# Kernel optimization log

Hardware: AMD Instinct MI355X
Metric: run time of the kernel (lower is better)

Reference implementation:

```python
import jax, jax.numpy as jnp
import numpy as np

B, IN_CH, OUT_CH, ZDIM, KSZ, WH = 16, 64, 64, 64, 3, 32
T, K = 32768, 128


def setup_inputs() -> dict:
    key = jax.random.key(0)
    ks = jax.random.split(key, 10)
    bound = float(np.sqrt(6.0 / OUT_CH))
    return {
        "x": jax.random.normal(ks[0], (B, IN_CH, T), jnp.float32),
        "z": jax.random.normal(ks[1], (B, ZDIM, K), jnp.float32),
        # weight_model: conv1x1(ZDIM->WH), ReLU, conv1x1(WH->IN_CH*OUT_CH*KSZ)
        "wm1": jax.random.normal(ks[2], (WH, ZDIM), jnp.float32) * 0.1,
        "wb1": jnp.zeros((WH,), jnp.float32),
        "wm2": jax.random.normal(ks[3], (IN_CH * OUT_CH * KSZ, WH), jnp.float32) * 0.02,
        "wb2": jnp.zeros((IN_CH * OUT_CH * KSZ,), jnp.float32),
        # bias_model: conv1x1(ZDIM->WH), ReLU, conv1x1(WH->OUT_CH)
        "bm1": jax.random.normal(ks[4], (WH, ZDIM), jnp.float32) * 0.1,
        "bb1": jnp.zeros((WH,), jnp.float32),
        "bm2": jax.random.normal(ks[5], (OUT_CH, WH), jnp.float32) * 0.1,
        "bb2": jnp.zeros((OUT_CH,), jnp.float32),
        # residual / skip 1x1 convs (uniform init per module)
        "rw": jax.random.uniform(ks[6], (OUT_CH, OUT_CH), jnp.float32, -bound, bound),
        "rb": jnp.zeros((OUT_CH,), jnp.float32),
        "sw": jax.random.uniform(ks[7], (OUT_CH, OUT_CH), jnp.float32, -bound, bound),
        "sb": jnp.zeros((OUT_CH,), jnp.float32),
    }


def reference(x, z, wm1, wb1, wm2, wb2, bm1, bb1, bm2, bb2, rw, rb, sw, sb):
    Bq, Cin, Tq = x.shape
    Kq = z.shape[-1]
    S = Tq // Kq  # samples per segment

    # hypernet: per-segment weights, shape (B, Cin*KSZ*OUT_CH, K)
    h = jax.nn.relu(jnp.einsum('hz,bzk->bhk', wm1, z) + wb1[None, :, None])
    w = jnp.einsum('oh,bhk->bok', wm2, h) + wb2[None, :, None]
    # (B, Cin*KSZ, OUT_CH, K) -> (B, K, KSZ, Cin, OUT_CH)
    w = w.reshape(Bq, KSZ, Cin, OUT_CH, Kq).transpose(0, 4, 1, 2, 3)
    # torch cat concatenates KSZ identical copies of x along channels (the
    # dilation shifts are absent in the source), so summing the weight over
    w_eff = w.sum(axis=2)  # (B, K, Cin, OUT_CH)

    hb = jax.nn.relu(jnp.einsum('hz,bzk->bhk', bm1, z) + bb1[None, :, None])
    b = jnp.einsum('oh,bhk->bok', bm2, hb) + bb2[None, :, None]  # (B, OUT_CH, K)
    b = b.transpose(0, 2, 1)  # (B, K, OUT_CH)

    # per-segment batched matmul
    xr = x.transpose(0, 2, 1).reshape(Bq, Kq, S, Cin)
    y = jnp.einsum('bksi,bkio->bkso', xr, w_eff) + b[:, :, None, :]
    y = jnp.sin(y.reshape(Bq, Tq, OUT_CH).transpose(0, 2, 1))  # (B, OUT_CH, T)

    residual = jnp.einsum('oc,bct->bot', rw, y) + rb[None, :, None]
    skip = jnp.einsum('oc,bct->bot', sw, y) + sb[None, :, None]
    return (residual + x) / 2, skip
```

## Files before the change

kernel.cpp:

```cpp
#include <hip/hip_runtime.h>
#include <hip/hip_bf16.h>

#define B_    16
#define CIN   64
#define COUT  64
#define ZD    64
#define WHID  32
#define TT    32768
#define KK    128
#define SS    256

__global__ void k_tapsum(const float* __restrict__ wm2, float* __restrict__ wm2s) {
    int i = blockIdx.x * 256 + threadIdx.x;
    if (i < 4096 * 32)
        wm2s[i] = wm2[i] + wm2[i + 131072] + wm2[i + 262144];
}

__global__ __launch_bounds__(256) void k_hyper_small(
    const float* __restrict__ z,
    const float* __restrict__ wm1, const float* __restrict__ wb1,
    const float* __restrict__ bm1, const float* __restrict__ bb1,
    const float* __restrict__ bm2, const float* __restrict__ bb2,
    float* __restrict__ ws_h, float* __restrict__ ws_bias)
{
    __shared__ float hb[8][32];
    const int tid = threadIdx.x;
    const int seg = tid >> 5, w = tid & 31;
    const int bk = blockIdx.x * 8 + seg;
    const int b = bk >> 7, k = bk & 127;
    const float* zp = z + b * ZD * KK + k;

    float hv = wb1[w], hbv = bb1[w];
    #pragma unroll
    for (int zz = 0; zz < 64; ++zz) {
        float zv = zp[zz * KK];
        hv  += wm1[w * 64 + zz] * zv;
        hbv += bm1[w * 64 + zz] * zv;
    }
    hv  = fmaxf(hv, 0.f);
    hbv = fmaxf(hbv, 0.f);
    ws_h[bk * 32 + w] = hv;
    hb[seg][w] = hbv;
    __syncthreads();

    #pragma unroll
    for (int t = 0; t < 2; ++t) {
        int o = w + t * 32;
        float acc = bb2[o];
        #pragma unroll
        for (int hh = 0; hh < 32; ++hh)
            acc += bm2[o * 32 + hh] * hb[seg][hh];
        ws_bias[bk * 64 + o] = acc;
    }
}

__global__ __launch_bounds__(256) void k_weff(
    const float* __restrict__ wm2s, const float* __restrict__ wb2,
    const float* __restrict__ ws_h, float* __restrict__ ws_w)
{
    const int tid = threadIdx.x;
    const int wave = tid >> 6, lane = tid & 63;
    const int bk0 = blockIdx.x * 16 + wave * 4;

    float hreg[4][32];
    #pragma unroll
    for (int q = 0; q < 4; ++q) {
        #pragma unroll
        for (int hh = 0; hh < 32; ++hh)
            hreg[q][hh] = ws_h[(bk0 + q) * 32 + hh];
    }

    for (int jj = 0; jj < 64; ++jj) {
        int j = jj * 64 + lane;
        float4 row[8];
        const float4* rp = (const float4*)(wm2s + j * 32);
        #pragma unroll
        for (int q = 0; q < 8; ++q) row[q] = rp[q];
        float wb = wb2[j] + wb2[j + 4096] + wb2[j + 8192];
        const float* rowf = (const float*)row;
        #pragma unroll
        for (int q = 0; q < 4; ++q) {
            float acc = wb;
            #pragma unroll
            for (int hh = 0; hh < 32; ++hh)
                acc += rowf[hh] * hreg[q][hh];
            ws_w[(size_t)(bk0 + q) * 4096 + j] = acc;
        }
    }
}

__global__ __launch_bounds__(256, 2) void k_main(
    const float* __restrict__ x,
    const float* __restrict__ ws_w, const float* __restrict__ ws_bias,
    const float* __restrict__ rw, const float* __restrict__ rb,
    const float* __restrict__ sw, const float* __restrict__ sb,
    float* __restrict__ out)
{
    __shared__ float U[8192];
    __shared__ unsigned short ybuf[64][256];

    const int tid = threadIdx.x;
    const int bk = blockIdx.x;
    const int b = bk >> 7, k = bk & 127;
    const int tbase = k * SS;
    const int sg = tid & 63, og = tid >> 6;
    const int s0 = sg * 4, o0 = og * 16;
    float4* U4 = (float4*)U;

    {
        const float4* Wg = (const float4*)(ws_w + (size_t)bk * 4096);
        #pragma unroll
        for (int r = 0; r < 4; ++r) U4[tid + 256 * r] = Wg[tid + 256 * r];
        if (tid < 64) U[4096 + tid] = ws_bias[bk * 64 + tid];
    }
    __syncthreads();

    float acc[4][16];
    #pragma unroll
    for (int e = 0; e < 4; ++e)
        #pragma unroll
        for (int v = 0; v < 16; ++v) acc[e][v] = 0.f;

    const float* xs = x + (size_t)b * CIN * TT + tbase + s0;
    #pragma unroll 8
    for (int i = 0; i < 64; ++i) {
        float4 xv = *(const float4*)(xs + (size_t)i * TT);
        #pragma unroll
        for (int q = 0; q < 4; ++q) {
            float4 wq = U4[i * 16 + og * 4 + q];
            float wv[4] = {wq.x, wq.y, wq.z, wq.w};
            #pragma unroll
            for (int e2 = 0; e2 < 4; ++e2) {
                acc[0][q * 4 + e2] += xv.x * wv[e2];
                acc[1][q * 4 + e2] += xv.y * wv[e2];
                acc[2][q * 4 + e2] += xv.z * wv[e2];
                acc[3][q * 4 + e2] += xv.w * wv[e2];
            }
        }
    }
    #pragma unroll
    for (int v = 0; v < 16; ++v) {
        int o = o0 + v;
        float bo = U[4096 + o];
        unsigned int us[4];
        #pragma unroll
        for (int e = 0; e < 4; ++e) {
            float yv = __sinf(acc[e][v] + bo);
            unsigned int u = __float_as_uint(yv);
            u += 0x7fffu + ((u >> 16) & 1u);
            us[e] = u >> 16;
        }
        uint2 pk;
        pk.x = us[0] | (us[1] << 16);
        pk.y = us[2] | (us[3] << 16);
        *(uint2*)&ybuf[o][s0] = pk;
    }
    __syncthreads();

    #pragma unroll
    for (int r = 0; r < 16; ++r) {
        int e = tid + 256 * r;
        int o = e >> 6, c = e & 63;
        U[c * 64 + o]        = rw[e];
        U[4096 + c * 64 + o] = sw[e];
    }
    __syncthreads();

    float ar[4][16], asx[4][16];
    #pragma unroll
    for (int e = 0; e < 4; ++e)
        #pragma unroll
        for (int v = 0; v < 16; ++v) { ar[e][v] = 0.f; asx[e][v] = 0.f; }

    #pragma unroll 4
    for (int c = 0; c < 64; ++c) {
        uint2 yu = *(const uint2*)&ybuf[c][s0];
        float yv[4];
        yv[0] = __uint_as_float(yu.x << 16);
        yv[1] = __uint_as_float(yu.x & 0xffff0000u);
        yv[2] = __uint_as_float(yu.y << 16);
        yv[3] = __uint_as_float(yu.y & 0xffff0000u);
        #pragma unroll
        for (int q = 0; q < 4; ++q) {
            float4 rq = U4[c * 16 + og * 4 + q];
            float4 sq = U4[1024 + c * 16 + og * 4 + q];
            float rv[4] = {rq.x, rq.y, rq.z, rq.w};
            float sv[4] = {sq.x, sq.y, sq.z, sq.w};
            #pragma unroll
            for (int e2 = 0; e2 < 4; ++e2) {
                #pragma unroll
                for (int e = 0; e < 4; ++e) {
                    ar[e][q * 4 + e2]  += yv[e] * rv[e2];
                    asx[e][q * 4 + e2] += yv[e] * sv[e2];
                }
            }
        }
    }

    float* resp = out;
    float* skpp = out + (size_t)B_ * COUT * TT;
    #pragma unroll
    for (int v = 0; v < 16; ++v) {
        int o = o0 + v;
        size_t off = (size_t)(b * COUT + o) * TT + tbase + s0;
        float4 xo = *(const float4*)(x + off);
        float rbv = rb[o], sbv = sb[o];
        float4 ro, so;
        ro.x = (ar[0][v] + rbv + xo.x) * 0.5f;
        ro.y = (ar[1][v] + rbv + xo.y) * 0.5f;
        ro.z = (ar[2][v] + rbv + xo.z) * 0.5f;
        ro.w = (ar[3][v] + rbv + xo.w) * 0.5f;
        so.x = asx[0][v] + sbv;
        so.y = asx[1][v] + sbv;
        so.z = asx[2][v] + sbv;
        so.w = asx[3][v] + sbv;
        *(float4*)(resp + off) = ro;
        *(float4*)(skpp + off) = so;
    }
}

extern "C" void kernel_launch(void* const* d_in, const int* in_sizes, int n_in,
                              void* d_out, int out_size, void* d_ws, size_t ws_size,
                              hipStream_t stream) {
    const float* x   = (const float*)d_in[0];
    const float* z   = (const float*)d_in[1];
    const float* wm1 = (const float*)d_in[2];
    const float* wb1 = (const float*)d_in[3];
    const float* wm2 = (const float*)d_in[4];
    const float* wb2 = (const float*)d_in[5];
    const float* bm1 = (const float*)d_in[6];
    const float* bb1 = (const float*)d_in[7];
    const float* bm2 = (const float*)d_in[8];
    const float* bb2 = (const float*)d_in[9];
    const float* rw  = (const float*)d_in[10];
    const float* rb  = (const float*)d_in[11];
    const float* sw  = (const float*)d_in[12];
    const float* sb  = (const float*)d_in[13];
    float* out = (float*)d_out;

    float* ws      = (float*)d_ws;
    float* ws_wm2s = ws;
    float* ws_h    = ws + 131072;
    float* ws_bias = ws + 196608;
    float* ws_w    = ws + 327680;

    hipLaunchKernelGGL(k_tapsum, dim3(512), dim3(256), 0, stream, wm2, ws_wm2s);
    hipLaunchKernelGGL(k_hyper_small, dim3(256), dim3(256), 0, stream,
                       z, wm1, wb1, bm1, bb1, bm2, bb2, ws_h, ws_bias);
    hipLaunchKernelGGL(k_weff, dim3(128), dim3(256), 0, stream,
                       ws_wm2s, wb2, ws_h, ws_w);
    hipLaunchKernelGGL(k_main, dim3(2048), dim3(256), 0, stream,
                       x, ws_w, ws_bias, rw, rb, sw, sb, out);
}
```

Before: 596.3 us.

## Stage x through LDS with cooperative prefetch and packed FMA accumulation

After: 1.027 ms. +72.2%, slower.

```diff
diff --git a/kernel.cpp b/kernel.cpp
--- a/kernel.cpp
+++ b/kernel.cpp
@@ -9,6 +9,9 @@
 #define TT    32768
 #define KK    128
 #define SS    256
+
+typedef float f2 __attribute__((ext_vector_type(2)));
+typedef float f4 __attribute__((ext_vector_type(4)));
 
 __global__ void k_tapsum(const float* __restrict__ wm2, float* __restrict__ wm2s) {
     int i = blockIdx.x * 256 + threadIdx.x;
@@ -97,7 +100,7 @@
     float* __restrict__ out)
 {
     __shared__ float U[8192];
-    __shared__ unsigned short ybuf[64][256];
+    __shared__ __align__(16) unsigned short ybuf[64][256];
 
     const int tid = threadIdx.x;
     const int bk = blockIdx.x;
@@ -105,39 +108,73 @@
     const int tbase = k * SS;
     const int sg = tid & 63, og = tid >> 6;
     const int s0 = sg * 4, o0 = og * 16;
-    float4* U4 = (float4*)U;
+    f4* U4 = (f4*)U;
+    f4* xch = (f4*)&ybuf[0][0];
 
     {
-        const float4* Wg = (const float4*)(ws_w + (size_t)bk * 4096);
+        const f4* Wg = (const f4*)(ws_w + (size_t)bk * 4096);
         #pragma unroll
         for (int r = 0; r < 4; ++r) U4[tid + 256 * r] = Wg[tid + 256 * r];
         if (tid < 64) U[4096 + tid] = ws_bias[bk * 64 + tid];
     }
-    __syncthreads();
-
-    float acc[4][16];
+
+    const float* xg = x + (size_t)b * CIN * TT + tbase + s0;
+    f4 pend0 = *(const f4*)(xg + (size_t)(0  + og) * TT);
+    f4 pend1 = *(const f4*)(xg + (size_t)(4  + og) * TT);
+    f4 pend2 = *(const f4*)(xg + (size_t)(8  + og) * TT);
+    f4 pend3 = *(const f4*)(xg + (size_t)(12 + og) * TT);
+    xch[og * 64 + sg] = pend0;
+
+    f2 acc[4][8];
     #pragma unroll
     for (int e = 0; e < 4; ++e)
         #pragma unroll
-        for (int v = 0; v < 16; ++v) acc[e][v] = 0.f;
-
-    const float* xs = x + (size_t)b * CIN * TT + tbase + s0;
-    #pragma unroll 8
-    for (int i = 0; i < 64; ++i) {
-        float4 xv = *(const float4*)(xs + (size_t)i * TT);
-        #pragma unroll
-        for (int q = 0; q < 4; ++q) {
-            float4 wq = U4[i * 16 + og * 4 + q];
-            float wv[4] = {wq.x, wq.y, wq.z, wq.w};
+        for (int p = 0; p < 8; ++p) { f2 z = {0.f, 0.f}; acc[e][p] = z; }
+
+    #pragma unroll 4
+    for (int j = 0; j < 16; ++j) {
+        __syncthreads();
+        if (j + 4 < 16) {
+            f4 v = *(const f4*)(xg + (size_t)((j + 4) * 4 + og) * TT);
+            if      (((j + 4) & 3) == 0) pend0 = v;
+            else if (((j + 4) & 3) == 1) pend1 = v;
+            else if (((j + 4) & 3) == 2) pend2 = v;
+            else                         pend3 = v;
+        }
+        #pragma unroll
+        for (int i = 0; i < 4; ++i) {
+            f4 xv = xch[(j & 1) * 256 + i * 64 + sg];
+            const int c = j * 4 + i;
+            f2 xs0 = xv.xx, xs1 = xv.yy, xs2 = xv.zz, xs3 = xv.ww;
             #pragma unroll
-            for (int e2 = 0; e2 < 4; ++e2) {
-                acc[0][q * 4 + e2] += xv.x * wv[e2];
-                acc[1][q * 4 + e2] += xv.y * wv[e2];
-                acc[2][q * 4 + e2] += xv.z * wv[e2];
-                acc[3][q * 4 + e2] += xv.w * wv[e2];
+            for (int q = 0; q < 4; ++q) {
+                f4 wq = U4[c * 16 + og * 4 + q];
+                f2 w0 = wq.xy, w1 = wq.zw;
+                acc[0][2*q]   += xs0 * w0;  acc[0][2*q+1] += xs0 * w1;
+                acc[1][2*q]   += xs1 * w0;  acc[1][2*q+1] += xs1 * w1;
+                acc[2][2*q]   += xs2 * w0;  acc[2][2*q+1] += xs2 * w1;
+                acc[3][2*q]   += xs3 * w0;  acc[3][2*q+1] += xs3 * w1;
             }
         }
-    }
+        if (j + 1 < 16) {
+            f4 w;
+            if      (((j + 1) & 3) == 0) w = pend0;
+            else if (((j + 1) & 3) == 1) w = pend1;
+            else if (((j + 1) & 3) == 2) w = pend2;
+            else                         w = pend3;
+            xch[((j + 1) & 1) * 256 + og * 64 + sg] = w;
+        }
+    }
+    __syncthreads();
+
+    float rgv[16], sgv[16];
+    #pragma unroll
+    for (int r = 0; r < 16; ++r) {
+        int idx = r * 256 + tid;
+        rgv[r] = rw[(idx & 63) * 64 + (idx >> 6)];
+        sgv[r] = sw[(idx & 63) * 64 + (idx >> 6)];
+    }
+
     #pragma unroll
     for (int v = 0; v < 16; ++v) {
         int o = o0 + v;
@@ -145,7 +182,7 @@
         unsigned int us[4];
         #pragma unroll
         for (int e = 0; e < 4; ++e) {
-            float yv = __sinf(acc[e][v] + bo);
+            float yv = __sinf(acc[e][v >> 1][v & 1] + bo);
             unsigned int u = __float_as_uint(yv);
             u += 0x7fffu + ((u >> 16) & 1u);
             us[e] = u >> 16;
@@ -159,41 +196,41 @@
 
     #pragma unroll
     for (int r = 0; r < 16; ++r) {
-        int e = tid + 256 * r;
-        int o = e >> 6, c = e & 63;
-        U[c * 64 + o]        = rw[e];
-        U[4096 + c * 64 + o] = sw[e];
-    }
-    __syncthreads();
-
-    float ar[4][16], asx[4][16];
+        int idx = r * 256 + tid;
+        int o = idx & 63, c = idx >> 6;
+        U[c * 64 + o]        = rgv[r];
+        U[4096 + c * 64 + o] = sgv[r];
+    }
+    __syncthreads();
+
+    f2 ar[4][8], as_[4][8];
     #pragma unroll
     for (int e = 0; e < 4; ++e)
         #pragma unroll
-        for (int v = 0; v < 16; ++v) { ar[e][v] = 0.f; asx[e][v] = 0.f; }
+        for (int p = 0; p < 8; ++p) { f2 z = {0.f, 0.f}; ar[e][p] = z; as_[e][p] = z; }
 
     #pragma unroll 4
     for (int c = 0; c < 64; ++c) {
         uint2 yu = *(const uint2*)&ybuf[c][s0];
-        float yv[4];
-        yv[0] = __uint_as_float(yu.x << 16);
-        yv[1] = __uint_as_float(yu.x & 0xffff0000u);
-        yv[2] = __uint_as_float(yu.y << 16);
-        yv[3] = __uint_as_float(yu.y & 0xffff0000u);
+        float y0 = __uint_as_float(yu.x << 16);
+        float y1 = __uint_as_float(yu.x & 0xffff0000u);
+        float y2 = __uint_as_float(yu.y << 16);
+        float y3 = __uint_as_float(yu.y & 0xffff0000u);
+        f2 d0 = {y0, y0}, d1 = {y1, y1}, d2 = {y2, y2}, d3 = {y3, y3};
         #pragma unroll
         for (int q = 0; q < 4; ++q) {
-            float4 rq = U4[c * 16 + og * 4 + q];
-            float4 sq = U4[1024 + c * 16 + og * 4 + q];
-            float rv[4] = {rq.x, rq.y, rq.z, rq.w};
-            float sv[4] = {sq.x, sq.y, sq.z, sq.w};
-            #pragma unroll
-            for (int e2 = 0; e2 < 4; ++e2) {
-                #pragma unroll
-                for (int e = 0; e < 4; ++e) {
-                    ar[e][q * 4 + e2]  += yv[e] * rv[e2];
-                    asx[e][q * 4 + e2] += yv[e] * sv[e2];
-                }
-            }
+            f4 rq = U4[c * 16 + og * 4 + q];
+            f4 sq = U4[1024 + c * 16 + og * 4 + q];
+            f2 r0 = rq.xy, r1 = rq.zw;
+            f2 v0 = sq.xy, v1 = sq.zw;
+            ar[0][2*q]  += d0 * r0;  ar[0][2*q+1]  += d0 * r1;
+            ar[1][2*q]  += d1 * r0;  ar[1][2*q+1]  += d1 * r1;
+            ar[2][2*q]  += d2 * r0;  ar[2][2*q+1]  += d2 * r1;
+            ar[3][2*q]  += d3 * r0;  ar[3][2*q+1]  += d3 * r1;
+            as_[0][2*q] += d0 * v0;  as_[0][2*q+1] += d0 * v1;
+            as_[1][2*q] += d1 * v0;  as_[1][2*q+1] += d1 * v1;
+            as_[2][2*q] += d2 * v0;  as_[2][2*q+1] += d2 * v1;
+            as_[3][2*q] += d3 * v0;  as_[3][2*q+1] += d3 * v1;
         }
     }
 
@@ -206,14 +243,14 @@
         float4 xo = *(const float4*)(x + off);
         float rbv = rb[o], sbv = sb[o];
         float4 ro, so;
-        ro.x = (ar[0][v] + rbv + xo.x) * 0.5f;
-        ro.y = (ar[1][v] + rbv + xo.y) * 0.5f;
-        ro.z = (ar[2][v] + rbv + xo.z) * 0.5f;
-        ro.w = (ar[3][v] + rbv + xo.w) * 0.5f;
-        so.x = asx[0][v] + sbv;
-        so.y = asx[1][v] + sbv;
-        so.z = asx[2][v] + sbv;
-        so.w = asx[3][v] + sbv;
+        ro.x = (ar[0][v >> 1][v & 1] + rbv + xo.x) * 0.5f;
+        ro.y = (ar[1][v >> 1][v & 1] + rbv + xo.y) * 0.5f;
+        ro.z = (ar[2][v >> 1][v & 1] + rbv + xo.z) * 0.5f;
+        ro.w = (ar[3][v >> 1][v & 1] + rbv + xo.w) * 0.5f;
+        so.x = as_[0][v >> 1][v & 1] + sbv;
+        so.y = as_[1][v >> 1][v & 1] + sbv;
+        so.z = as_[2][v >> 1][v & 1] + sbv;
+        so.w = as_[3][v >> 1][v & 1] + sbv;
         *(float4*)(resp + off) = ro;
         *(float4*)(skpp + off) = so;
     }
```

## Double k_main threads per segment, split k_weff per-segment, prefetch rw/sw into registers

Applied to the files above, without the earlier changes.

After: 648.3 us. 1.09x slower.

```diff
diff --git a/kernel.cpp b/kernel.cpp
--- a/kernel.cpp
+++ b/kernel.cpp
@@ -60,15 +60,12 @@
 {
     const int tid = threadIdx.x;
     const int wave = tid >> 6, lane = tid & 63;
-    const int bk0 = blockIdx.x * 16 + wave * 4;
-
-    float hreg[4][32];
-    #pragma unroll
-    for (int q = 0; q < 4; ++q) {
-        #pragma unroll
-        for (int hh = 0; hh < 32; ++hh)
-            hreg[q][hh] = ws_h[(bk0 + q) * 32 + hh];
-    }
+    const int bk = blockIdx.x * 4 + wave;
+
+    float hreg[32];
+    #pragma unroll
+    for (int hh = 0; hh < 32; ++hh)
+        hreg[hh] = ws_h[bk * 32 + hh];
 
     for (int jj = 0; jj < 64; ++jj) {
         int j = jj * 64 + lane;
@@ -78,18 +75,15 @@
         for (int q = 0; q < 8; ++q) row[q] = rp[q];
         float wb = wb2[j] + wb2[j + 4096] + wb2[j + 8192];
         const float* rowf = (const float*)row;
-        #pragma unroll
-        for (int q = 0; q < 4; ++q) {
-            float acc = wb;
-            #pragma unroll
-            for (int hh = 0; hh < 32; ++hh)
-                acc += rowf[hh] * hreg[q][hh];
-            ws_w[(size_t)(bk0 + q) * 4096 + j] = acc;
-        }
-    }
-}
-
-__global__ __launch_bounds__(256, 2) void k_main(
+        float acc = wb;
+        #pragma unroll
+        for (int hh = 0; hh < 32; ++hh)
+            acc += rowf[hh] * hreg[hh];
+        ws_w[(size_t)bk * 4096 + j] = acc;
+    }
+}
+
+__global__ __launch_bounds__(512, 4) void k_main(
     const float* __restrict__ x,
     const float* __restrict__ ws_w, const float* __restrict__ ws_bias,
     const float* __restrict__ rw, const float* __restrict__ rb,
@@ -97,37 +91,37 @@
     float* __restrict__ out)
 {
     __shared__ float U[8192];
-    __shared__ unsigned short ybuf[64][256];
+    __shared__ __align__(16) unsigned short ybuf[64][256];
 
     const int tid = threadIdx.x;
     const int bk = blockIdx.x;
     const int b = bk >> 7, k = bk & 127;
     const int tbase = k * SS;
     const int sg = tid & 63, og = tid >> 6;
-    const int s0 = sg * 4, o0 = og * 16;
+    const int s0 = sg * 4, o0 = og * 8;
     float4* U4 = (float4*)U;
 
     {
         const float4* Wg = (const float4*)(ws_w + (size_t)bk * 4096);
         #pragma unroll
-        for (int r = 0; r < 4; ++r) U4[tid + 256 * r] = Wg[tid + 256 * r];
+        for (int r = 0; r < 2; ++r) U4[tid + 512 * r] = Wg[tid + 512 * r];
         if (tid < 64) U[4096 + tid] = ws_bias[bk * 64 + tid];
     }
     __syncthreads();
 
-    float acc[4][16];
+    float acc[4][8];
     #pragma unroll
     for (int e = 0; e < 4; ++e)
         #pragma unroll
-        for (int v = 0; v < 16; ++v) acc[e][v] = 0.f;
+        for (int v = 0; v < 8; ++v) acc[e][v] = 0.f;
 
     const float* xs = x + (size_t)b * CIN * TT + tbase + s0;
     #pragma unroll 8
     for (int i = 0; i < 64; ++i) {
         float4 xv = *(const float4*)(xs + (size_t)i * TT);
         #pragma unroll
-        for (int q = 0; q < 4; ++q) {
-            float4 wq = U4[i * 16 + og * 4 + q];
+        for (int q = 0; q < 2; ++q) {
+            float4 wq = U4[i * 16 + og * 2 + q];
             float wv[4] = {wq.x, wq.y, wq.z, wq.w};
             #pragma unroll
             for (int e2 = 0; e2 < 4; ++e2) {
@@ -138,8 +132,18 @@
             }
         }
     }
-    #pragma unroll
-    for (int v = 0; v < 16; ++v) {
+
+    float rgv[8], sgv[8];
+    #pragma unroll
+    for (int r = 0; r < 8; ++r) {
+        int idx = r * 512 + tid;
+        int o = idx & 63, c = idx >> 6;
+        rgv[r] = rw[o * 64 + c];
+        sgv[r] = sw[o * 64 + c];
+    }
+
+    #pragma unroll
+    for (int v = 0; v < 8; ++v) {
         int o = o0 + v;
         float bo = U[4096 + o];
         unsigned int us[4];
@@ -158,19 +162,19 @@
     __syncthreads();
 
     #pragma unroll
-    for (int r = 0; r < 16; ++r) {
-        int e = tid + 256 * r;
-        int o = e >> 6, c = e & 63;
-        U[c * 64 + o]        = rw[e];
-        U[4096 + c * 64 + o] = sw[e];
-    }
-    __syncthreads();
-
-    float ar[4][16], asx[4][16];
+    for (int r = 0; r < 8; ++r) {
+        int idx = r * 512 + tid;
+        int o = idx & 63, c = idx >> 6;
+        U[c * 64 + o]        = rgv[r];
+        U[4096 + c * 64 + o] = sgv[r];
+    }
+    __syncthreads();
+
+    float ar[4][8], asx[4][8];
     #pragma unroll
     for (int e = 0; e < 4; ++e)
         #pragma unroll
-        for (int v = 0; v < 16; ++v) { ar[e][v] = 0.f; asx[e][v] = 0.f; }
+        for (int v = 0; v < 8; ++v) { ar[e][v] = 0.f; asx[e][v] = 0.f; }
 
     #pragma unroll 4
     for (int c = 0; c < 64; ++c) {
@@ -181,9 +185,9 @@
         yv[2] = __uint_as_float(yu.y << 16);
         yv[3] = __uint_as_float(yu.y & 0xffff0000u);
         #pragma unroll
-        for (int q = 0; q < 4; ++q) {
-            float4 rq = U4[c * 16 + og * 4 + q];
-            float4 sq = U4[1024 + c * 16 + og * 4 + q];
+        for (int q = 0; q < 2; ++q) {
+            float4 rq = U4[c * 16 + og * 2 + q];
+            float4 sq = U4[1024 + c * 16 + og * 2 + q];
             float rv[4] = {rq.x, rq.y, rq.z, rq.w};
             float sv[4] = {sq.x, sq.y, sq.z, sq.w};
             #pragma unroll
@@ -200,7 +204,7 @@
     float* resp = out;
     float* skpp = out + (size_t)B_ * COUT * TT;
     #pragma unroll
-    for (int v = 0; v < 16; ++v) {
+    for (int v = 0; v < 8; ++v) {
         int o = o0 + v;
         size_t off = (size_t)(b * COUT + o) * TT + tbase + s0;
         float4 xo = *(const float4*)(x + off);
@@ -247,8 +251,8 @@
     hipLaunchKernelGGL(k_tapsum, dim3(512), dim3(256), 0, stream, wm2, ws_wm2s);
     hipLaunchKernelGGL(k_hyper_small, dim3(256), dim3(256), 0, stream,
                        z, wm1, wb1, bm1, bb1, bm2, bb2, ws_h, ws_bias);
-    hipLaunchKernelGGL(k_weff, dim3(128), dim3(256), 0, stream,
+    hipLaunchKernelGGL(k_weff, dim3(512), dim3(256), 0, stream,
                        ws_wm2s, wb2, ws_h, ws_w);
-    hipLaunchKernelGGL(k_main, dim3(2048), dim3(256), 0, stream,
+    hipLaunchKernelGGL(k_main, dim3(2048), dim3(512), 0, stream,
                        x, ws_w, ws_bias, rw, rb, sw, sb, out);
 }
```
